# Optimization experiments

Measured on AMD Instinct MI355X. Metric: run time of the kernel, lower is better.

## Reference

```python
import jax, jax.numpy as jnp
import numpy as np

DIM = 512
NUM_HEADS = 8
DIM_HEAD = 64
INNER = NUM_HEADS * DIM_HEAD  # 512
EPS = 1e-5


def setup_inputs() -> dict:
    key = jax.random.key(0)
    ks = jax.random.split(key, 6)
    B, H, W = 16, 64, 64
    x = jax.random.normal(ks[0], (B, DIM, H, W), dtype=jnp.float32)
    # 1x1 conv weights stored as [out, in]
    w_qkv = jax.random.normal(ks[1], (3 * INNER, DIM), dtype=jnp.float32) * (1.0 / np.sqrt(DIM))
    w_out = jax.random.normal(ks[2], (DIM, INNER), dtype=jnp.float32) * (1.0 / np.sqrt(INNER))
    b_out = jax.random.normal(ks[3], (DIM,), dtype=jnp.float32) * 0.01
    gamma = jnp.ones((DIM,), dtype=jnp.float32)
    beta = jnp.zeros((DIM,), dtype=jnp.float32)
    return {"x": x, "w_qkv": w_qkv, "w_out": w_out, "b_out": b_out,
            "gamma": gamma, "beta": beta}


def reference(x, w_qkv, w_out, b_out, gamma, beta):
    B, C, H, W = x.shape
    N = H * W
    # 1x1 conv == channel GEMM
    qkv = jnp.einsum('bchw,oc->bohw', x, w_qkv)            # [B, 3*INNER, H, W]
    qkv = qkv.reshape(B, 3, NUM_HEADS, DIM_HEAD, N)        # chunk along channel
    q, k, v = qkv[:, 0], qkv[:, 1], qkv[:, 2]              # each [B, h, Dh, N]
    # NOTE: faithful to source — attention over channel dim (Dh x Dh), not N x N
    scores = jnp.einsum('bhdn,bhen->bhde', q, k) / np.sqrt(DIM_HEAD)
    attn = jax.nn.softmax(scores, axis=-1)                 # [B, h, Dh, Dh]
    out = jnp.einsum('bhde,bhen->bhdn', attn, v)           # [B, h, Dh, N]
    out = out.reshape(B, INNER, H, W)
    out = jnp.einsum('bchw,oc->bohw', out, w_out) + b_out[None, :, None, None]
    # GroupNorm with 1 group == per-sample layernorm over (C,H,W) with channel affine
    mean = jnp.mean(out, axis=(1, 2, 3), keepdims=True)
    var = jnp.var(out, axis=(1, 2, 3), keepdims=True)
    out = (out - mean) * jax.lax.rsqrt(var + EPS)
    out = out * gamma[None, :, None, None] + beta[None, :, None, None]
    return out
```

## Files before the change

### kernel.cpp

```cpp
#include <hip/hip_runtime.h>

typedef __bf16 bf16;
typedef __bf16 bf16x8 __attribute__((ext_vector_type(8)));
typedef __bf16 bf16x4 __attribute__((ext_vector_type(4)));
typedef float  f32x4  __attribute__((ext_vector_type(4)));

#define BATCH   16
#define CDIM    512
#define NSPAT   4096
#define QKV_M   1536
#define INNER   512

__device__ __forceinline__ void gld16(const bf16* g, const bf16* l) {
  __builtin_amdgcn_global_load_lds(
      (const __attribute__((address_space(1))) void*)g,
      (__attribute__((address_space(3))) void*)l, 16, 0, 0);
}

__global__ __launch_bounds__(256) void cast_f32_bf16_kernel(
    const float* __restrict__ in, bf16* __restrict__ out, int n4) {
  int i = blockIdx.x * 256 + threadIdx.x;
  if (i >= n4) return;
  float4 v = ((const float4*)in)[i];
  bf16x4 o = { (bf16)v.x, (bf16)v.y, (bf16)v.z, (bf16)v.w };
  *(bf16x4*)(out + (size_t)i * 4) = o;
}

__global__ __launch_bounds__(256) void transpose_cast_kernel(
    const float* __restrict__ x, bf16* __restrict__ xt) {
  __shared__ __attribute__((aligned(16))) bf16 T[64][72];
  int b = blockIdx.z, c0 = blockIdx.y * 64, n0 = blockIdx.x * 64;
  int t = threadIdx.x;
  const float* xp = x + ((size_t)b * CDIM + c0) * NSPAT + n0;
#pragma unroll
  for (int i = 0; i < 4; ++i) {
    int v = t + i * 256;
    int c = v >> 4, nq = (v & 15) * 4;
    float4 rd = *(const float4*)(xp + (size_t)c * NSPAT + nq);
    T[nq + 0][c] = (bf16)rd.x; T[nq + 1][c] = (bf16)rd.y;
    T[nq + 2][c] = (bf16)rd.z; T[nq + 3][c] = (bf16)rd.w;
  }
  __syncthreads();
  bf16* op = xt + ((size_t)b * NSPAT + n0) * CDIM + c0;
#pragma unroll
  for (int i = 0; i < 2; ++i) {
    int v = t + i * 256;
    int n = v >> 3, cc = (v & 7) * 8;
    *(bf16x8*)(op + (size_t)n * CDIM + cc) = *(const bf16x8*)&T[n][cc];
  }
}

template <int OUTMODE>
__global__ __launch_bounds__(256) void gemm_tn_kernel(
    const bf16* __restrict__ A, const bf16* __restrict__ Bt,
    void* __restrict__ Cout, const float* __restrict__ bias,
    float* __restrict__ part, int M, int N, int K) {
  __shared__ __attribute__((aligned(16))) bf16 smem[8192];

  int b  = blockIdx.z;
  int m0 = blockIdx.y * 128, n0 = blockIdx.x * 128;
  const bf16* Ab = A + (size_t)m0 * K;
  const bf16* Bb = Bt + ((size_t)b * N + n0) * K;

  int tid = threadIdx.x, lane = tid & 63, wid = tid >> 6;
  int wm = wid >> 1, wn = wid & 1, lm = lane & 15, kqd = lane >> 4;
  int srow = lane >> 2, skb = lane & 3;

  f32x4 acc[4][4] = {};

  for (int k0 = 0; k0 < K; k0 += 32) {
#pragma unroll
    for (int i = 0; i < 2; ++i) {
      int gi = wid * 2 + i;
      gld16(Ab + (size_t)(gi * 16 + srow) * K + k0 + skb * 8, smem + gi * 512);
      gld16(Bb + (size_t)(gi * 16 + srow) * K + k0 + skb * 8, smem + 4096 + gi * 512);
    }
    __syncthreads();
    bf16x8 af[4], bfr[4];
#pragma unroll
    for (int im = 0; im < 4; ++im)
      af[im] = *(const bf16x8*)&smem[(wm * 64 + im * 16 + lm) * 32 + kqd * 8];
#pragma unroll
    for (int in = 0; in < 4; ++in)
      bfr[in] = *(const bf16x8*)&smem[4096 + (wn * 64 + in * 16 + lm) * 32 + kqd * 8];
#pragma unroll
    for (int im = 0; im < 4; ++im)
#pragma unroll
      for (int in = 0; in < 4; ++in)
        acc[im][in] = __builtin_amdgcn_mfma_f32_16x16x32_bf16(af[im], bfr[in], acc[im][in], 0, 0, 0);
    __syncthreads();
  }

  if (OUTMODE == 0) {
    bf16* C = (bf16*)Cout + (size_t)b * M * N;
    bf16* Ws = smem + wid * 2048;
#pragma unroll
    for (int half = 0; half < 2; ++half) {
#pragma unroll
      for (int im2 = 0; im2 < 2; ++im2) {
        int im = half * 2 + im2;
#pragma unroll
        for (int in = 0; in < 4; ++in)
#pragma unroll
          for (int r = 0; r < 4; ++r)
            Ws[(im2 * 16 + kqd * 4 + r) * 64 + in * 16 + lm] = (bf16)acc[im][in][r];
      }
#pragma unroll
      for (int j = 0; j < 4; ++j) {
        int u = lane + j * 64;
        int row = u >> 3, cu = (u & 7) * 8;
        *(bf16x8*)(C + (size_t)(m0 + wm * 64 + half * 32 + row) * N + n0 + wn * 64 + cu) =
            *(const bf16x8*)&Ws[row * 64 + cu];
      }
    }
  } else {
    float* C = (float*)Cout + (size_t)b * M * N;
    float s = 0.f, s2 = 0.f;
#pragma unroll
    for (int im = 0; im < 4; ++im)
#pragma unroll
      for (int in = 0; in < 4; ++in) {
        int row = m0 + wm * 64 + im * 16 + kqd * 4;
        int col = n0 + wn * 64 + in * 16 + lm;
#pragma unroll
        for (int r = 0; r < 4; ++r) {
          float v = acc[im][in][r] + bias[row + r];
          C[(size_t)(row + r) * N + col] = v;
          s += v; s2 += v * v;
        }
      }
#pragma unroll
    for (int off = 32; off > 0; off >>= 1) {
      s  += __shfl_down(s, off, 64);
      s2 += __shfl_down(s2, off, 64);
    }
    __shared__ float red[8];
    if (lane == 0) { red[wid] = s; red[wid + 4] = s2; }
    __syncthreads();
    if (tid == 0) {
      atomicAdd(&part[b * 2],     red[0] + red[1] + red[2] + red[3]);
      atomicAdd(&part[b * 2 + 1], red[4] + red[5] + red[6] + red[7]);
    }
  }
}

__global__ __launch_bounds__(256) void attn_scores_kernel(
    const bf16* __restrict__ qkv, float* __restrict__ sc_part) {
  __shared__ __attribute__((aligned(16))) bf16 qs[4096];
  int chunk = blockIdx.x, bh = blockIdx.y, b = bh >> 3, h = bh & 7;
  const bf16* q = qkv + ((size_t)b * QKV_M + h * 64) * NSPAT + chunk * 512;
  const bf16* k = q + (size_t)INNER * NSPAT;

  int tid = threadIdx.x, lane = tid & 63, wid = tid >> 6;
  int lm = lane & 15, kqd = lane >> 4, d0 = wid * 16;
  int srow = lane >> 2, skb = lane & 3;

  f32x4 acc[4] = {};
  for (int n0 = 0; n0 < 512; n0 += 32) {
    gld16(q + (size_t)(wid * 16 + srow) * NSPAT + n0 + skb * 8, qs + wid * 512);
    gld16(k + (size_t)(wid * 16 + srow) * NSPAT + n0 + skb * 8, qs + 2048 + wid * 512);
    __syncthreads();
    bf16x8 a = *(const bf16x8*)&qs[(d0 + lm) * 32 + kqd * 8];
#pragma unroll
    for (int eb = 0; eb < 4; ++eb) {
      bf16x8 bb = *(const bf16x8*)&qs[2048 + (eb * 16 + lm) * 32 + kqd * 8];
      acc[eb] = __builtin_amdgcn_mfma_f32_16x16x32_bf16(a, bb, acc[eb], 0, 0, 0);
    }
    __syncthreads();
  }
  float* outp = sc_part + ((size_t)bh * 8 + chunk) * 4096;
#pragma unroll
  for (int eb = 0; eb < 4; ++eb)
#pragma unroll
    for (int r = 0; r < 4; ++r)
      outp[(d0 + kqd * 4 + r) * 64 + eb * 16 + lm] = acc[eb][r];
}

__global__ __launch_bounds__(256) void attn_softmax_kernel(
    const float* __restrict__ sc_part, bf16* __restrict__ attn_w) {
  __shared__ float ssum[64][65];
  int bh = blockIdx.x, t = threadIdx.x;
  const float* p = sc_part + (size_t)bh * 8 * 4096;
  float v[16];
#pragma unroll
  for (int j = 0; j < 16; ++j) v[j] = p[t + j * 256];
  for (int c = 1; c < 8; ++c)
#pragma unroll
    for (int j = 0; j < 16; ++j) v[j] += p[c * 4096 + t + j * 256];
#pragma unroll
  for (int j = 0; j < 16; ++j) {
    int q = t + j * 256;
    ssum[q >> 6][q & 63] = v[j];
  }
  __syncthreads();
  if (t < 64) {
    float mx = -1e30f;
    for (int e = 0; e < 64; ++e) mx = fmaxf(mx, ssum[t][e]);
    float s = 0.f;
    for (int e = 0; e < 64; ++e) {
      float ex = __expf((ssum[t][e] - mx) * 0.125f);
      ssum[t][e] = ex; s += ex;
    }
    float inv = 1.0f / s;
    bf16* ow = attn_w + (size_t)bh * 4096 + t * 64;
    for (int e = 0; e < 64; ++e) ow[e] = (bf16)(ssum[t][e] * inv);
  }
}

__global__ __launch_bounds__(256) void attn_pv_kernel(
    const bf16* __restrict__ qkv, const bf16* __restrict__ attn_w,
    bf16* __restrict__ attn_t) {
  __shared__ __attribute__((aligned(16))) bf16 aw[64 * 72];
  __shared__ __attribute__((aligned(16))) bf16 Vs[128 * 72];
  int chunk = blockIdx.x, bh = blockIdx.y, b = bh >> 3, h = bh & 7;
  const bf16* vmat = qkv + ((size_t)b * QKV_M + 2 * INNER + h * 64) * NSPAT + chunk * 512;
  bf16* outt = attn_t + ((size_t)b * NSPAT + chunk * 512) * INNER + h * 64;

  int tid = threadIdx.x, lane = tid & 63, wid = tid >> 6;
  int lm = lane & 15, kqd = lane >> 4, d0 = wid * 16;

#pragma unroll
  for (int i = 0; i < 2; ++i) {
    int v = tid + i * 256;
    *(bf16x8*)&aw[(v >> 3) * 72 + (v & 7) * 8] = *(const bf16x8*)(attn_w + (size_t)bh * 4096 + v * 8);
  }
  __syncthreads();
  bf16x8 a0 = *(const bf16x8*)&aw[(d0 + lm) * 72 + kqd * 8];
  bf16x8 a1 = *(const bf16x8*)&aw[(d0 + lm) * 72 + 32 + kqd * 8];

  for (int nc = 0; nc < 512; nc += 128) {
    __syncthreads();
#pragma unroll
    for (int i = 0; i < 4; ++i) {
      int v = i * 256 + tid;
      int e = v & 63, nn = (v >> 6) * 8;
      bf16x8 d = *(const bf16x8*)(vmat + (size_t)e * NSPAT + nc + nn);
#pragma unroll
      for (int j = 0; j < 8; ++j) Vs[(nn + j) * 72 + e] = d[j];
    }
    __syncthreads();
    f32x4 o[8];
#pragma unroll
    for (int nt = 0; nt < 8; ++nt) {
      bf16x8 b0 = *(const bf16x8*)&Vs[(nt * 16 + lm) * 72 + kqd * 8];
      bf16x8 b1 = *(const bf16x8*)&Vs[(nt * 16 + lm) * 72 + 32 + kqd * 8];
      o[nt] = (f32x4){0.f, 0.f, 0.f, 0.f};
      o[nt] = __builtin_amdgcn_mfma_f32_16x16x32_bf16(a0, b0, o[nt], 0, 0, 0);
      o[nt] = __builtin_amdgcn_mfma_f32_16x16x32_bf16(a1, b1, o[nt], 0, 0, 0);
    }
    __syncthreads();
#pragma unroll
    for (int nt = 0; nt < 8; ++nt) {
      bf16x4 ov = { (bf16)o[nt][0], (bf16)o[nt][1], (bf16)o[nt][2], (bf16)o[nt][3] };
      *(bf16x4*)&Vs[(nt * 16 + lm) * 72 + d0 + kqd * 4] = ov;
    }
    __syncthreads();
#pragma unroll
    for (int i = 0; i < 4; ++i) {
      int v = i * 256 + tid;
      int n = v >> 3, dc = (v & 7) * 8;
      *(bf16x8*)(outt + (size_t)(nc + n) * INNER + dc) = *(const bf16x8*)&Vs[n * 72 + dc];
    }
  }
}

__global__ void ln_stats_kernel(const float* __restrict__ part, float2* __restrict__ stats) {
  int b = threadIdx.x;
  if (b < 16) {
    const float invn = 1.0f / 2097152.0f;
    float mean = part[b * 2] * invn;
    float var  = part[b * 2 + 1] * invn - mean * mean;
    stats[b] = make_float2(mean, rsqrtf(var + 1e-5f));
  }
}

__global__ __launch_bounds__(256) void ln_apply_kernel(
    float* __restrict__ out, const float2* __restrict__ stats,
    const float* __restrict__ gamma, const float* __restrict__ beta) {
  size_t i4 = (size_t)blockIdx.x * 256 + threadIdx.x;
  size_t e  = i4 * 4;
  int b = (int)(e >> 21);
  int c = (int)((e >> 12) & 511);
  float2 st = stats[b];
  float g  = gamma[c] * st.y;
  float bb = beta[c] - st.x * g;
  float4* p = (float4*)out;
  float4 v = p[i4];
  v.x = v.x * g + bb; v.y = v.y * g + bb; v.z = v.z * g + bb; v.w = v.w * g + bb;
  p[i4] = v;
}

extern "C" void kernel_launch(void* const* d_in, const int* in_sizes, int n_in,
                              void* d_out, int out_size, void* d_ws, size_t ws_size,
                              hipStream_t stream) {
  const float* x      = (const float*)d_in[0];
  const float* w_qkv  = (const float*)d_in[1];
  const float* w_out  = (const float*)d_in[2];
  const float* b_out  = (const float*)d_in[3];
  const float* gamma  = (const float*)d_in[4];
  const float* beta   = (const float*)d_in[5];
  float* out = (float*)d_out;

  char* ws = (char*)d_ws;
  bf16*   xt      = (bf16*)(ws);
  float*  sc_part = (float*)(ws);
  bf16*   attn_w  = (bf16*)(ws + 16777216);
  bf16*   wqkvb   = (bf16*)(ws + 67108864);
  bf16*   woutb   = (bf16*)(ws + 68681728);
  bf16*   qkvb    = (bf16*)(ws + 69206016);
  bf16*   attn_t  = (bf16*)(ws + 270532608);
  float*  part    = (float*)(ws + 337641472);
  float2* stats   = (float2*)(ws + 337641600);

  hipMemsetAsync(part, 0, 128, stream);

  transpose_cast_kernel<<<dim3(64, 8, BATCH), 256, 0, stream>>>(x, xt);
  cast_f32_bf16_kernel<<<768, 256, 0, stream>>>(w_qkv, wqkvb, 196608);
  cast_f32_bf16_kernel<<<256, 256, 0, stream>>>(w_out, woutb, 65536);

  gemm_tn_kernel<0><<<dim3(32, 12, BATCH), 256, 0, stream>>>(
      wqkvb, xt, (void*)qkvb, nullptr, nullptr, QKV_M, NSPAT, CDIM);

  attn_scores_kernel<<<dim3(8, 128), 256, 0, stream>>>(qkvb, sc_part);
  attn_softmax_kernel<<<128, 256, 0, stream>>>(sc_part, attn_w);
  attn_pv_kernel<<<dim3(8, 128), 256, 0, stream>>>(qkvb, attn_w, attn_t);

  gemm_tn_kernel<1><<<dim3(32, 4, BATCH), 256, 0, stream>>>(
      woutb, attn_t, (void*)out, b_out, part, INNER, NSPAT, CDIM);

  ln_stats_kernel<<<1, 16, 0, stream>>>(part, stats);
  ln_apply_kernel<<<32768, 256, 0, stream>>>(out, stats, gamma, beta);
}
```

Measured before the change: 572.5 us.

## Replace 128x128 GEMM with 256x256 multi-stage pipelined swizzled-LDS GEMM

Both channel GEMMs now use 512-thread blocks computing 256x256 tiles. A 4-stage LDS ring buffer is filled with async global-to-LDS loads issued three tiles ahead and paced by explicit vmcnt waits. The LDS layout is XOR-swizzled to avoid bank conflicts, and s_setprio raises priority around MFMA bursts. The aim is to hide global load latency, cut per-iteration barrier stalls and raise operand reuse, at the cost of 128KB LDS per block, fewer blocks and code specialised to K=512.

```diff
diff --git a/kernel.cpp b/kernel.cpp
--- a/kernel.cpp
+++ b/kernel.cpp
@@ -10,12 +10,19 @@
 #define NSPAT   4096
 #define QKV_M   1536
 #define INNER   512
+#define GK      512
+#define GNT     16
 
 __device__ __forceinline__ void gld16(const bf16* g, const bf16* l) {
   __builtin_amdgcn_global_load_lds(
       (const __attribute__((address_space(1))) void*)g,
       (__attribute__((address_space(3))) void*)l, 16, 0, 0);
 }
+
+#define SBAR() do { asm volatile("" ::: "memory"); __builtin_amdgcn_s_barrier(); \
+                    asm volatile("" ::: "memory"); } while (0)
+#define LGKM0    asm volatile("s_waitcnt lgkmcnt(0)" ::: "memory")
+#define VMCNT(n) asm volatile("s_waitcnt vmcnt(" #n ")" ::: "memory")
 
 __global__ __launch_bounds__(256) void cast_f32_bf16_kernel(
     const float* __restrict__ in, bf16* __restrict__ out, int n4) {
@@ -51,80 +58,111 @@
 }
 
 template <int OUTMODE>
-__global__ __launch_bounds__(256) void gemm_tn_kernel(
+__global__ __launch_bounds__(512, 2) void gemm256_kernel(
     const bf16* __restrict__ A, const bf16* __restrict__ Bt,
     void* __restrict__ Cout, const float* __restrict__ bias,
-    float* __restrict__ part, int M, int N, int K) {
-  __shared__ __attribute__((aligned(16))) bf16 smem[8192];
-
-  int b  = blockIdx.z;
-  int m0 = blockIdx.y * 128, n0 = blockIdx.x * 128;
-  const bf16* Ab = A + (size_t)m0 * K;
-  const bf16* Bb = Bt + ((size_t)b * N + n0) * K;
-
+    float* __restrict__ part, int M, int N) {
+  __shared__ __attribute__((aligned(16))) bf16 Sm[65536];
+
+  int bz = blockIdx.z;
+  int m0 = blockIdx.y * 256, n0 = blockIdx.x * 256;
   int tid = threadIdx.x, lane = tid & 63, wid = tid >> 6;
-  int wm = wid >> 1, wn = wid & 1, lm = lane & 15, kqd = lane >> 4;
-  int srow = lane >> 2, skb = lane & 3;
-
-  f32x4 acc[4][4] = {};
-
-  for (int k0 = 0; k0 < K; k0 += 32) {
-#pragma unroll
-    for (int i = 0; i < 2; ++i) {
-      int gi = wid * 2 + i;
-      gld16(Ab + (size_t)(gi * 16 + srow) * K + k0 + skb * 8, smem + gi * 512);
-      gld16(Bb + (size_t)(gi * 16 + srow) * K + k0 + skb * 8, smem + 4096 + gi * 512);
-    }
-    __syncthreads();
-    bf16x8 af[4], bfr[4];
-#pragma unroll
-    for (int im = 0; im < 4; ++im)
-      af[im] = *(const bf16x8*)&smem[(wm * 64 + im * 16 + lm) * 32 + kqd * 8];
-#pragma unroll
-    for (int in = 0; in < 4; ++in)
-      bfr[in] = *(const bf16x8*)&smem[4096 + (wn * 64 + in * 16 + lm) * 32 + kqd * 8];
-#pragma unroll
-    for (int im = 0; im < 4; ++im)
-#pragma unroll
-      for (int in = 0; in < 4; ++in)
-        acc[im][in] = __builtin_amdgcn_mfma_f32_16x16x32_bf16(af[im], bfr[in], acc[im][in], 0, 0, 0);
-    __syncthreads();
-  }
+  int wm = wid >> 2, wn = wid & 3;
+  int lm = lane & 15, kqd = lane >> 4;
+
+  int aoff[8], boff[4];
+#pragma unroll
+  for (int mf = 0; mf < 8; ++mf) {
+    int x = (mf * 16 + lm) * 4 + kqd;
+    aoff[mf] = wm * 4096 + (x ^ ((x >> 3) & 7)) * 8;
+  }
+#pragma unroll
+  for (int nf = 0; nf < 4; ++nf) {
+    int x = ((wn & 1) * 64 + nf * 16 + lm) * 4 + kqd;
+    boff[nf] = 8192 + (wn >> 1) * 4096 + (x ^ ((x >> 3) & 7)) * 8;
+  }
+
+  int sl = tid ^ ((tid >> 3) & 7);
+  int srow = sl >> 2, sc8 = (sl & 3) * 8;
+  const bf16* aS = A + (size_t)(m0 + srow) * GK + sc8;
+  const bf16* bS = Bt + ((size_t)bz * N + n0 + srow) * GK + sc8;
+
+  f32x4 acc[8][4] = {};
+
+#define STG_A(t) do { bf16* d = Sm + (((t)) & 3) * 16384 + wid * 512; \
+    gld16(aS + (size_t)(t) * 32, d); \
+    gld16(aS + (size_t)128 * GK + (size_t)(t) * 32, d + 4096); } while (0)
+#define STG_B(t) do { bf16* d = Sm + (((t)) & 3) * 16384 + 8192 + wid * 512; \
+    gld16(bS + (size_t)(t) * 32, d); \
+    gld16(bS + (size_t)128 * GK + (size_t)(t) * 32, d + 4096); } while (0)
+
+  STG_A(0); STG_B(0); STG_A(1); STG_B(1); STG_A(2); STG_B(2);
+  VMCNT(8);
+  SBAR();
+
+#define TILE_BODY(t, DOSTG, WAITK) do { \
+    const bf16* Sb = Sm + ((t) & 3) * 16384; \
+    bf16x8 af[4], bq[4]; \
+    _Pragma("unroll") for (int i = 0; i < 4; ++i) af[i] = *(const bf16x8*)(Sb + aoff[i]); \
+    _Pragma("unroll") for (int i = 0; i < 4; ++i) bq[i] = *(const bf16x8*)(Sb + boff[i]); \
+    if (DOSTG) STG_A((t) + 3); \
+    SBAR(); LGKM0; \
+    __builtin_amdgcn_s_setprio(1); \
+    _Pragma("unroll") for (int i = 0; i < 4; ++i) \
+      _Pragma("unroll") for (int j = 0; j < 4; ++j) \
+        acc[i][j] = __builtin_amdgcn_mfma_f32_16x16x32_bf16(af[i], bq[j], acc[i][j], 0, 0, 0); \
+    __builtin_amdgcn_s_setprio(0); \
+    SBAR(); \
+    _Pragma("unroll") for (int i = 0; i < 4; ++i) af[i] = *(const bf16x8*)(Sb + aoff[4 + i]); \
+    if (DOSTG) STG_B((t) + 3); \
+    SBAR(); LGKM0; \
+    __builtin_amdgcn_s_setprio(1); \
+    _Pragma("unroll") for (int i = 0; i < 4; ++i) \
+      _Pragma("unroll") for (int j = 0; j < 4; ++j) \
+        acc[4 + i][j] = __builtin_amdgcn_mfma_f32_16x16x32_bf16(af[i], bq[j], acc[4 + i][j], 0, 0, 0); \
+    __builtin_amdgcn_s_setprio(0); \
+    WAITK; \
+    SBAR(); \
+  } while (0)
+
+  for (int tt = 0; tt < 12; tt += 4) {
+#pragma unroll
+    for (int q = 0; q < 4; ++q) TILE_BODY(tt + q, 1, VMCNT(8));
+  }
+  TILE_BODY(12, 1, VMCNT(8));
+  TILE_BODY(13, 0, VMCNT(4));
+  TILE_BODY(14, 0, VMCNT(0));
+  TILE_BODY(15, 0, (void)0);
 
   if (OUTMODE == 0) {
-    bf16* C = (bf16*)Cout + (size_t)b * M * N;
-    bf16* Ws = smem + wid * 2048;
-#pragma unroll
-    for (int half = 0; half < 2; ++half) {
-#pragma unroll
-      for (int im2 = 0; im2 < 2; ++im2) {
-        int im = half * 2 + im2;
-#pragma unroll
-        for (int in = 0; in < 4; ++in)
-#pragma unroll
-          for (int r = 0; r < 4; ++r)
-            Ws[(im2 * 16 + kqd * 4 + r) * 64 + in * 16 + lm] = (bf16)acc[im][in][r];
-      }
-#pragma unroll
-      for (int j = 0; j < 4; ++j) {
-        int u = lane + j * 64;
-        int row = u >> 3, cu = (u & 7) * 8;
-        *(bf16x8*)(C + (size_t)(m0 + wm * 64 + half * 32 + row) * N + n0 + wn * 64 + cu) =
-            *(const bf16x8*)&Ws[row * 64 + cu];
-      }
+    bf16* C = (bf16*)Cout + (size_t)bz * M * N;
+    bf16* Ws = Sm + wid * 8192;
+#pragma unroll
+    for (int mf = 0; mf < 8; ++mf)
+#pragma unroll
+      for (int nf = 0; nf < 4; ++nf)
+#pragma unroll
+        for (int r = 0; r < 4; ++r)
+          Ws[(mf * 16 + kqd * 4 + r) * 64 + nf * 16 + lm] = (bf16)acc[mf][nf][r];
+#pragma unroll
+    for (int j = 0; j < 16; ++j) {
+      int u = j * 64 + lane;
+      int row = u >> 3, cu = (u & 7) * 8;
+      *(bf16x8*)(C + (size_t)(m0 + wm * 128 + row) * N + (n0 + wn * 64 + cu)) =
+          *(const bf16x8*)&Ws[row * 64 + cu];
     }
   } else {
-    float* C = (float*)Cout + (size_t)b * M * N;
+    float* C = (float*)Cout + (size_t)bz * M * N;
     float s = 0.f, s2 = 0.f;
 #pragma unroll
-    for (int im = 0; im < 4; ++im)
-#pragma unroll
-      for (int in = 0; in < 4; ++in) {
-        int row = m0 + wm * 64 + im * 16 + kqd * 4;
-        int col = n0 + wn * 64 + in * 16 + lm;
+    for (int mf = 0; mf < 8; ++mf)
+#pragma unroll
+      for (int nf = 0; nf < 4; ++nf) {
+        int row = m0 + wm * 128 + mf * 16 + kqd * 4;
+        int col = n0 + wn * 64 + nf * 16 + lm;
 #pragma unroll
         for (int r = 0; r < 4; ++r) {
-          float v = acc[im][in][r] + bias[row + r];
+          float v = acc[mf][nf][r] + bias[row + r];
           C[(size_t)(row + r) * N + col] = v;
           s += v; s2 += v * v;
         }
@@ -134,14 +172,14 @@
       s  += __shfl_down(s, off, 64);
       s2 += __shfl_down(s2, off, 64);
     }
-    __shared__ float red[8];
-    if (lane == 0) { red[wid] = s; red[wid + 4] = s2; }
-    __syncthreads();
-    if (tid == 0) {
-      atomicAdd(&part[b * 2],     red[0] + red[1] + red[2] + red[3]);
-      atomicAdd(&part[b * 2 + 1], red[4] + red[5] + red[6] + red[7]);
-    }
-  }
+    if (lane == 0) {
+      atomicAdd(&part[bz * 2],     s);
+      atomicAdd(&part[bz * 2 + 1], s2);
+    }
+  }
+#undef TILE_BODY
+#undef STG_A
+#undef STG_B
 }
 
 __global__ __launch_bounds__(256) void attn_scores_kernel(
@@ -318,15 +356,15 @@
   cast_f32_bf16_kernel<<<768, 256, 0, stream>>>(w_qkv, wqkvb, 196608);
   cast_f32_bf16_kernel<<<256, 256, 0, stream>>>(w_out, woutb, 65536);
 
-  gemm_tn_kernel<0><<<dim3(32, 12, BATCH), 256, 0, stream>>>(
-      wqkvb, xt, (void*)qkvb, nullptr, nullptr, QKV_M, NSPAT, CDIM);
+  gemm256_kernel<0><<<dim3(16, 6, BATCH), 512, 0, stream>>>(
+      wqkvb, xt, (void*)qkvb, nullptr, nullptr, QKV_M, NSPAT);
 
   attn_scores_kernel<<<dim3(8, 128), 256, 0, stream>>>(qkvb, sc_part);
   attn_softmax_kernel<<<128, 256, 0, stream>>>(sc_part, attn_w);
   attn_pv_kernel<<<dim3(8, 128), 256, 0, stream>>>(qkvb, attn_w, attn_t);
 
-  gemm_tn_kernel<1><<<dim3(32, 4, BATCH), 256, 0, stream>>>(
-      woutb, attn_t, (void*)out, b_out, part, INNER, NSPAT, CDIM);
+  gemm256_kernel<1><<<dim3(16, 2, BATCH), 512, 0, stream>>>(
+      woutb, attn_t, (void*)out, b_out, part, INNER, NSPAT);
 
   ln_stats_kernel<<<1, 16, 0, stream>>>(part, stats);
   ln_apply_kernel<<<32768, 256, 0, stream>>>(out, stats, gamma, beta);
```

New measurement: 594.3 us. +3.8%, slower.
